# Kernel tuning notes

Hardware: AMD Instinct MI355X
Metric: run time of the kernel (lower is better)

The kernel has to match this reference:

```python
import jax, jax.numpy as jnp
import numpy as np
import math

B, L, S, H, E, D = 4, 2048, 2048, 8, 64, 64


def setup_inputs() -> dict:
    key = jax.random.key(0)
    kq, kk, kv = jax.random.split(key, 3)
    queries = jax.random.normal(kq, (B, L, H, E), dtype=jnp.float32)
    keys = jax.random.normal(kk, (B, S, H, E), dtype=jnp.float32)
    values = jax.random.normal(kv, (B, S, H, D), dtype=jnp.float32)
    # TriangularCausalMask: True above the diagonal = masked out
    attn_mask = jnp.triu(jnp.ones((L, S), dtype=bool), k=1)[None, None]  # [1,1,L,S]
    return {"queries": queries, "keys": keys, "values": values, "attn_mask": attn_mask}


def reference(queries, keys, values, attn_mask):
    # queries [B,L,H,E], keys [B,S,H,E], values [B,S,H,D], attn_mask bool [1,1,L,S]
    scale = 1.0 / math.sqrt(queries.shape[-1])
    scores = jnp.einsum('blhe,bshe->bhls', queries, keys)  # [B,H,L,S]
    scores = jnp.where(attn_mask, -jnp.inf, scores)
    A = jax.nn.softmax(scale * scores, axis=-1)  # dropout p=0.0 -> identity
    V = jnp.einsum('bhls,bshd->blhd', A, values)  # [B,L,H,D]
    return V
```

## Files before the change

kernel.cpp:

```cpp
#include <hip/hip_runtime.h>


typedef unsigned short u16;
typedef unsigned int   u32;
typedef short short8   __attribute__((ext_vector_type(8)));
typedef float floatx16 __attribute__((ext_vector_type(16)));
typedef u32 u32x4      __attribute__((ext_vector_type(4)));

#define B_ 4
#define L_ 2048
#define S_ 2048
#define H_ 8
#define E_ 64
#define D_ 64

static __device__ __forceinline__ u32 pack2(float lo, float hi) {
    const u32 a = __float_as_uint(lo) + 0x8000u;
    const u32 b = __float_as_uint(hi) + 0x8000u;
    return __builtin_amdgcn_perm(b, a, 0x07060302u);
}
static __device__ __forceinline__ u16 bf16c(float x) {
    return (u16)((__float_as_uint(x) + 0x8000u) >> 16);
}
static __device__ __forceinline__ void pl32swap(u32& a, u32& b) {
    asm("v_permlane32_swap_b32 %0, %1" : "+v"(a), "+v"(b));
}
static __device__ __forceinline__ floatx16 zero16() {
    floatx16 z;
    #pragma unroll
    for (int i = 0; i < 16; i++) z[i] = 0.f;
    return z;
}

__global__ __launch_bounds__(256)
void cvt_kernel(const float* __restrict__ k, const float* __restrict__ v,
                u16* __restrict__ kc, u16* __restrict__ vt)
{
    __shared__ u16 Lt[64 * 72];
    const int bx = blockIdx.x, t = threadIdx.x;
    const int tile = bx & 1023;
    const int kt = tile & 31, h = (tile >> 5) & 7, b = tile >> 8;
    const int F  = t >> 5;
    const int hi = (t >> 4) & 1;
    const int l0 = (t & 15) * 2;

    if (bx < 1024) {
        const int mt = F >> 2, ks = F & 3;
        const int s  = kt * 64 + mt * 32 + l0;
        const int e  = ks * 16 + hi * 8;
        const float* p0 = k + (((size_t)(b * S_ + s)) * H_ + h) * E_ + e;
        const float4 a0 = ((const float4*)p0)[0], a1 = ((const float4*)p0)[1];
        const float* p1 = p0 + H_ * E_;
        const float4 b0 = ((const float4*)p1)[0], b1 = ((const float4*)p1)[1];
        u16* dst = kc + ((size_t)(b * 8 + h)) * 131072 + (size_t)kt * 4096 + t * 16;
        *(u32x4*)dst = (u32x4){pack2(a0.x, a0.y), pack2(a0.z, a0.w),
                               pack2(a1.x, a1.y), pack2(a1.z, a1.w)};
        *(u32x4*)(dst + 8) = (u32x4){pack2(b0.x, b0.y), pack2(b0.z, b0.w),
                                     pack2(b1.x, b1.y), pack2(b1.z, b1.w)};
    } else {
        {
            const int i  = t >> 2;
            const int d0 = (t & 3) * 16;
            const float* vp = v + (((size_t)(b * S_ + kt * 64 + i)) * H_ + h) * D_ + d0;
            const float4 a0 = ((const float4*)vp)[0], a1 = ((const float4*)vp)[1];
            const float4 a2 = ((const float4*)vp)[2], a3 = ((const float4*)vp)[3];
            const float va[16] = {a0.x,a0.y,a0.z,a0.w, a1.x,a1.y,a1.z,a1.w,
                                  a2.x,a2.y,a2.z,a2.w, a3.x,a3.y,a3.z,a3.w};
            #pragma unroll
            for (int jj = 0; jj < 16; jj++) Lt[(d0 + jj) * 72 + i] = bf16c(va[jj]);
        }
        __syncthreads();
        {
            const int nt = F >> 2, ks = F & 3;
            const int d1 = nt * 32 + l0;
            u16* dst = vt + ((size_t)(b * 8 + h)) * 131072 + (size_t)kt * 4096 + t * 16;
            *(u32x4*)dst       = *(const u32x4*)&Lt[(d1    ) * 72 + ks * 16 + hi * 8];
            *(u32x4*)(dst + 8) = *(const u32x4*)&Lt[(d1 + 1) * 72 + ks * 16 + hi * 8];
        }
    }
}

template<int SRC>
__global__ __launch_bounds__(128, 2)
void fa_kernel(const float* __restrict__ q, const float* __restrict__ kk,
               const float* __restrict__ vv, const u16* __restrict__ kc,
               const u16* __restrict__ vt, float* __restrict__ out)
{
    __shared__ float Ls[64 * 33 + 128];

    const int tid  = threadIdx.x;
    const int w    = tid >> 6;
    const int lane = tid & 63;
    const int l31  = lane & 31;
    const int hi   = lane >> 5;

    const int bx = blockIdx.x;
    int h, b, s32, kt0, ktend;
    bool split, diag;
    if (bx < 1024) {
        split = true;
        h = bx & 7; b = (bx >> 3) & 3;
        s32 = 63 - (bx >> 5);
        const int klast = s32 >> 1;
        const int mid   = (klast + 1) >> 1;
        if (w == 0) { kt0 = 0;   ktend = mid - 1; diag = false; }
        else        { kt0 = mid; ktend = klast;   diag = true;  }
    } else {
        split = false; diag = true;
        const int idx = bx - 1024;
        h = idx & 7; b = (idx >> 3) & 3;
        const int jj = idx >> 5;
        s32 = w ? jj : (31 - jj);
        kt0 = 0; ktend = s32 >> 1;
    }
    const int q0 = s32 * 32;

    const float kscale = 0.18033688011112042f;

    const float* qptr = q + (((size_t)b * L_ + q0 + l31) * H_ + h) * E_ + hi * 8;
    short8 qf[4];
    #pragma unroll
    for (int ks = 0; ks < 4; ks++) {
        const float4 a0 = *(const float4*)(qptr + ks * 16);
        const float4 a1 = *(const float4*)(qptr + ks * 16 + 4);
        const u32x4 u = {pack2(a0.x * kscale, a0.y * kscale), pack2(a0.z * kscale, a0.w * kscale),
                         pack2(a1.x * kscale, a1.y * kscale), pack2(a1.z * kscale, a1.w * kscale)};
        qf[ks] = __builtin_bit_cast(short8, u);
    }

    const size_t bh = (size_t)(b * 8 + h);
    const u16* kcb = kc + bh * 131072;
    const u16* vtb = vt + bh * 131072;

    auto loadK = [&](int kt, int mt, int ks) -> short8 {
        if constexpr (SRC == 0) {
            const u32x4 u = *(const u32x4*)&kcb[(size_t)kt * 4096 + (mt * 4 + ks) * 512 + lane * 8];
            return __builtin_bit_cast(short8, u);
        } else {
            const float* p = kk + (((size_t)b * S_ + kt * 64 + mt * 32 + l31) * H_ + h) * E_ + ks * 16 + hi * 8;
            const float4 a0 = *(const float4*)p;
            const float4 a1 = *(const float4*)(p + 4);
            const u32x4 u = {pack2(a0.x, a0.y), pack2(a0.z, a0.w), pack2(a1.x, a1.y), pack2(a1.z, a1.w)};
            return __builtin_bit_cast(short8, u);
        }
    };
    auto loadV = [&](int kt, int nt, int ks) -> short8 {
        if constexpr (SRC == 0) {
            const u32x4 u = *(const u32x4*)&vtb[(size_t)kt * 4096 + (nt * 4 + ks) * 512 + lane * 8];
            return __builtin_bit_cast(short8, u);
        } else {
            float f[8];
            #pragma unroll
            for (int jj = 0; jj < 8; jj++)
                f[jj] = vv[(((size_t)b * S_ + kt * 64 + ks * 16 + hi * 8 + jj) * H_ + h) * D_ + nt * 32 + l31];
            const u32x4 u = {pack2(f[0], f[1]), pack2(f[2], f[3]), pack2(f[4], f[5]), pack2(f[6], f[7])};
            return __builtin_bit_cast(short8, u);
        }
    };

    floatx16 occ[2] = {zero16(), zero16()};
    float m_run = -1e30f, l_run = 0.f;

    short8 kf[2][4], vf[2][4];
    #pragma unroll
    for (int mt = 0; mt < 2; mt++)
        #pragma unroll
        for (int ks = 0; ks < 4; ks++) { kf[mt][ks] = loadK(kt0, mt, ks); vf[mt][ks] = loadV(kt0, mt, ks); }

    for (int kt = kt0; kt <= ktend; kt++) {
        floatx16 sac[2];
        __builtin_amdgcn_s_setprio(1);
        #pragma unroll
        for (int mt = 0; mt < 2; mt++) {
            floatx16 c = zero16();
            #pragma unroll
            for (int ks = 0; ks < 4; ks++)
                c = __builtin_amdgcn_mfma_f32_32x32x16_bf16(kf[mt][ks], qf[ks], c, 0, 0, 0);
            sac[mt] = c;
        }
        __builtin_amdgcn_s_setprio(0);

        if (kt < ktend) {
            #pragma unroll
            for (int mt = 0; mt < 2; mt++)
                #pragma unroll
                for (int ks = 0; ks < 4; ks++) kf[mt][ks] = loadK(kt + 1, mt, ks);
        }

        if (diag && kt == ktend) {
            const int qg = q0 + l31;
            #pragma unroll
            for (int mt = 0; mt < 2; mt++)
                #pragma unroll
                for (int r = 0; r < 16; r++) {
                    const int keyg = kt * 64 + mt * 32 + (r & 3) + (r >> 2) * 8 + hi * 4;
                    if (keyg > qg) sac[mt][r] = -1e30f;
                }
        }

        float red[16];
        #pragma unroll
        for (int r = 0; r < 16; r++) red[r] = fmaxf(sac[0][r], sac[1][r]);
        #pragma unroll
        for (int stp = 8; stp > 0; stp >>= 1)
            #pragma unroll
            for (int r = 0; r < stp; r++) red[r] = fmaxf(red[r], red[r + stp]);
        const float mx = fmaxf(red[0], __shfl_xor(red[0], 32));

        const bool defer = __all(mx - m_run <= 8.0f) != 0;
        if (!defer) {
            const float mnew  = fmaxf(m_run, mx);
            const float alpha = exp2f(m_run - mnew);
            m_run = mnew;
            l_run *= alpha;
            #pragma unroll
            for (int nt = 0; nt < 2; nt++)
                #pragma unroll
                for (int r = 0; r < 16; r++) occ[nt][r] *= alpha;
        }

        float sum[16];
        #pragma unroll
        for (int r = 0; r < 16; r++) {
            sac[0][r] = exp2f(sac[0][r] - m_run);
            sac[1][r] = exp2f(sac[1][r] - m_run);
            sum[r] = sac[0][r] + sac[1][r];
        }
        #pragma unroll
        for (int stp = 8; stp > 0; stp >>= 1)
            #pragma unroll
            for (int r = 0; r < stp; r++) sum[r] += sum[r + stp];
        l_run += sum[0] + __shfl_xor(sum[0], 32);

        u32 pk0[8], pk1[8];
        #pragma unroll
        for (int r2 = 0; r2 < 4; r2++) {
            pk0[r2 * 2 + 0] = pack2(sac[0][4 * r2 + 0], sac[0][4 * r2 + 1]);
            pk0[r2 * 2 + 1] = pack2(sac[0][4 * r2 + 2], sac[0][4 * r2 + 3]);
            pk1[r2 * 2 + 0] = pack2(sac[1][4 * r2 + 0], sac[1][4 * r2 + 1]);
            pk1[r2 * 2 + 1] = pack2(sac[1][4 * r2 + 2], sac[1][4 * r2 + 3]);
        }

        __builtin_amdgcn_s_setprio(1);
        #pragma unroll
        for (int ks = 0; ks < 4; ks++) {
            const int u = (ks & 1) * 4;
            u32 w0, w1, w2, w3;
            if (ks < 2) { w0 = pk0[u]; w1 = pk0[u + 1]; w2 = pk0[u + 2]; w3 = pk0[u + 3]; }
            else        { w0 = pk1[u]; w1 = pk1[u + 1]; w2 = pk1[u + 2]; w3 = pk1[u + 3]; }
            pl32swap(w0, w2);
            pl32swap(w1, w3);
            const u32x4 pw = {w0, w1, w2, w3};
            const short8 pf = __builtin_bit_cast(short8, pw);
            occ[0] = __builtin_amdgcn_mfma_f32_32x32x16_bf16(vf[0][ks], pf, occ[0], 0, 0, 0);
            occ[1] = __builtin_amdgcn_mfma_f32_32x32x16_bf16(vf[1][ks], pf, occ[1], 0, 0, 0);
        }
        __builtin_amdgcn_s_setprio(0);

        if (kt < ktend) {
            #pragma unroll
            for (int nt = 0; nt < 2; nt++)
                #pragma unroll
                for (int ks = 0; ks < 4; ks++) vf[nt][ks] = loadV(kt + 1, nt, ks);
        }
    }

    if (split) {
        if (w == 1) {
            #pragma unroll
            for (int nt = 0; nt < 2; nt++)
                #pragma unroll
                for (int r = 0; r < 16; r++) Ls[lane * 33 + nt * 16 + r] = occ[nt][r];
            Ls[2112 + lane] = m_run;
            Ls[2176 + lane] = l_run;
        }
        __syncthreads();
        if (w == 0) {
            const float mB = Ls[2112 + lane], lB = Ls[2176 + lane];
            const float m  = fmaxf(m_run, mB);
            const float aA = exp2f(m_run - m), aB = exp2f(mB - m);
            const float inv = 1.0f / (l_run * aA + lB * aB);
            float* op = out + (((size_t)b * L_ + q0 + l31) * H_ + h) * D_;
            #pragma unroll
            for (int nt = 0; nt < 2; nt++)
                #pragma unroll
                for (int r2 = 0; r2 < 4; r2++) {
                    const float4 o = {
                        (occ[nt][4 * r2 + 0] * aA + Ls[lane * 33 + nt * 16 + 4 * r2 + 0] * aB) * inv,
                        (occ[nt][4 * r2 + 1] * aA + Ls[lane * 33 + nt * 16 + 4 * r2 + 1] * aB) * inv,
                        (occ[nt][4 * r2 + 2] * aA + Ls[lane * 33 + nt * 16 + 4 * r2 + 2] * aB) * inv,
                        (occ[nt][4 * r2 + 3] * aA + Ls[lane * 33 + nt * 16 + 4 * r2 + 3] * aB) * inv};
                    *(float4*)(op + nt * 32 + r2 * 8 + hi * 4) = o;
                }
        }
    } else {
        const float inv = 1.0f / l_run;
        float* op = out + (((size_t)b * L_ + q0 + l31) * H_ + h) * D_;
        #pragma unroll
        for (int nt = 0; nt < 2; nt++)
            #pragma unroll
            for (int r2 = 0; r2 < 4; r2++) {
                const float4 o = {occ[nt][4 * r2 + 0] * inv, occ[nt][4 * r2 + 1] * inv,
                                  occ[nt][4 * r2 + 2] * inv, occ[nt][4 * r2 + 3] * inv};
                *(float4*)(op + nt * 32 + r2 * 8 + hi * 4) = o;
            }
    }
}

extern "C" void kernel_launch(void* const* d_in, const int* in_sizes, int n_in,
                              void* d_out, int out_size, void* d_ws, size_t ws_size,
                              hipStream_t stream) {
    const float* q = (const float*)d_in[0];
    const float* k = (const float*)d_in[1];
    const float* v = (const float*)d_in[2];
    float* out = (float*)d_out;

    const size_t elems = (size_t)B_ * H_ * S_ * E_;
    const size_t need  = elems * 2 * 2;
    if (d_ws != nullptr && ws_size >= need) {
        u16* kc = (u16*)d_ws;
        u16* vt = kc + elems;
        cvt_kernel<<<dim3(2048), dim3(256), 0, stream>>>(k, v, kc, vt);
        fa_kernel<0><<<dim3(1536), dim3(128), 0, stream>>>(q, k, v, kc, vt, out);
    } else {
        fa_kernel<1><<<dim3(1536), dim3(128), 0, stream>>>(q, k, v, nullptr, nullptr, out);
    }
}
```

Measured before the change: 153.4 us.

## Restructure flash-attention loop with K double-buffering, V in-tile loads, and occupancy 3

Rewrites the main KV loop as a two-way unrolled macro that ping-pongs between two K register buffers. V for the current tile and K for the next tile are issued together at the start of each step, with sched_barriers fencing the phases. The launch bound rises from 2 to 3 blocks per SM, the max and sum reductions become shallower trees, and the bf16 packing moves to the hardware v_cvt_pk_bf16_f32 instruction. Non-split blocks are re-paired so the two waves handle adjacent query tiles with equal trip counts. Risks include register spills under the tighter occupancy bound and V load latency now being exposed within the same step.

```diff
diff --git a/kernel.cpp b/kernel.cpp
--- a/kernel.cpp
+++ b/kernel.cpp
@@ -21,6 +21,11 @@
 }
 static __device__ __forceinline__ u16 bf16c(float x) {
     return (u16)((__float_as_uint(x) + 0x8000u) >> 16);
+}
+static __device__ __forceinline__ u32 cvtpk(float lo, float hi) {
+    u32 r;
+    asm("v_cvt_pk_bf16_f32 %0, %1, %2" : "=v"(r) : "v"(lo), "v"(hi));
+    return r;
 }
 static __device__ __forceinline__ void pl32swap(u32& a, u32& b) {
     asm("v_permlane32_swap_b32 %0, %1" : "+v"(a), "+v"(b));
@@ -80,8 +85,102 @@
     }
 }
 
+#define TILE_STEP(CURK, NXTK)                                                   \
+{                                                                               \
+    _Pragma("unroll")                                                           \
+    for (int ks = 0; ks < 4; ks++) {                                            \
+        vf[0][ks] = loadV(kt, 0, ks);                                           \
+        vf[1][ks] = loadV(kt, 1, ks);                                           \
+    }                                                                           \
+    if (kt < ktend) {                                                           \
+        _Pragma("unroll")                                                       \
+        for (int ks = 0; ks < 4; ks++) {                                        \
+            NXTK[0][ks] = loadK(kt + 1, 0, ks);                                 \
+            NXTK[1][ks] = loadK(kt + 1, 1, ks);                                 \
+        }                                                                       \
+    }                                                                           \
+    __builtin_amdgcn_sched_barrier(0);                                          \
+    floatx16 sac0, sac1;                                                        \
+    {                                                                           \
+        __builtin_amdgcn_s_setprio(1);                                          \
+        floatx16 c0 = zero16(), c1 = zero16();                                  \
+        _Pragma("unroll")                                                       \
+        for (int ks = 0; ks < 4; ks++) {                                        \
+            c0 = __builtin_amdgcn_mfma_f32_32x32x16_bf16(CURK[0][ks], qf[ks], c0, 0, 0, 0); \
+            c1 = __builtin_amdgcn_mfma_f32_32x32x16_bf16(CURK[1][ks], qf[ks], c1, 0, 0, 0); \
+        }                                                                       \
+        __builtin_amdgcn_s_setprio(0);                                          \
+        sac0 = c0; sac1 = c1;                                                   \
+    }                                                                           \
+    __builtin_amdgcn_sched_barrier(0);                                          \
+    if (diag && kt == ktend) {                                                  \
+        const int qg = q0 + l31;                                                \
+        _Pragma("unroll")                                                       \
+        for (int r = 0; r < 16; r++) {                                          \
+            const int key0 = kt * 64 + (r & 3) + (r >> 2) * 8 + hi * 4;         \
+            if (key0 > qg)      sac0[r] = -1e30f;                               \
+            if (key0 + 32 > qg) sac1[r] = -1e30f;                               \
+        }                                                                       \
+    }                                                                           \
+    float m01[8];                                                               \
+    _Pragma("unroll")                                                           \
+    for (int r = 0; r < 8; r++)                                                 \
+        m01[r] = fmaxf(fmaxf(sac0[r], sac0[r + 8]), fmaxf(sac1[r], sac1[r + 8])); \
+    const float t0  = fmaxf(fmaxf(m01[0], m01[1]), m01[2]);                     \
+    const float t1  = fmaxf(fmaxf(m01[3], m01[4]), m01[5]);                     \
+    const float t2  = fmaxf(fmaxf(m01[6], m01[7]), t0);                         \
+    const float mxl = fmaxf(t1, t2);                                            \
+    const float mx  = fmaxf(mxl, __shfl_xor(mxl, 32));                          \
+    const bool defer = __all(mx - m_run <= 8.0f) != 0;                          \
+    if (!defer) {                                                               \
+        const float mnew  = fmaxf(m_run, mx);                                   \
+        const float alpha = exp2f(m_run - mnew);                                \
+        m_run = mnew;                                                           \
+        l_run *= alpha;                                                         \
+        _Pragma("unroll")                                                       \
+        for (int r = 0; r < 16; r++) { occ[0][r] *= alpha; occ[1][r] *= alpha; } \
+    }                                                                           \
+    _Pragma("unroll")                                                           \
+    for (int r = 0; r < 16; r++) {                                              \
+        sac0[r] = exp2f(sac0[r] - m_run);                                       \
+        sac1[r] = exp2f(sac1[r] - m_run);                                       \
+    }                                                                           \
+    float sm[8];                                                                \
+    _Pragma("unroll")                                                           \
+    for (int r = 0; r < 8; r++)                                                 \
+        sm[r] = (sac0[r] + sac0[r + 8]) + (sac1[r] + sac1[r + 8]);              \
+    const float u0 = (sm[0] + sm[1]) + (sm[2] + sm[3]);                         \
+    const float u1 = (sm[4] + sm[5]) + (sm[6] + sm[7]);                         \
+    const float pssum = u0 + u1;                                                \
+    l_run += pssum + __shfl_xor(pssum, 32);                                     \
+    __builtin_amdgcn_sched_barrier(0);                                          \
+    u32 pk0[8], pk1[8];                                                         \
+    _Pragma("unroll")                                                           \
+    for (int r2 = 0; r2 < 4; r2++) {                                            \
+        pk0[2 * r2 + 0] = cvtpk(sac0[4 * r2 + 0], sac0[4 * r2 + 1]);            \
+        pk0[2 * r2 + 1] = cvtpk(sac0[4 * r2 + 2], sac0[4 * r2 + 3]);            \
+        pk1[2 * r2 + 0] = cvtpk(sac1[4 * r2 + 0], sac1[4 * r2 + 1]);            \
+        pk1[2 * r2 + 1] = cvtpk(sac1[4 * r2 + 2], sac1[4 * r2 + 3]);            \
+    }                                                                           \
+    __builtin_amdgcn_s_setprio(1);                                              \
+    _Pragma("unroll")                                                           \
+    for (int ks = 0; ks < 4; ks++) {                                            \
+        const int u = (ks & 1) * 4;                                             \
+        u32 w0, w1, w2, w3;                                                     \
+        if (ks < 2) { w0 = pk0[u]; w1 = pk0[u + 1]; w2 = pk0[u + 2]; w3 = pk0[u + 3]; } \
+        else        { w0 = pk1[u]; w1 = pk1[u + 1]; w2 = pk1[u + 2]; w3 = pk1[u + 3]; } \
+        pl32swap(w0, w2);                                                       \
+        pl32swap(w1, w3);                                                       \
+        const u32x4 pw = {w0, w1, w2, w3};                                      \
+        const short8 pf = __builtin_bit_cast(short8, pw);                       \
+        occ[0] = __builtin_amdgcn_mfma_f32_32x32x16_bf16(vf[0][ks], pf, occ[0], 0, 0, 0); \
+        occ[1] = __builtin_amdgcn_mfma_f32_32x32x16_bf16(vf[1][ks], pf, occ[1], 0, 0, 0); \
+    }                                                                           \
+    __builtin_amdgcn_s_setprio(0);                                              \
+}
+
 template<int SRC>
-__global__ __launch_bounds__(128, 2)
+__global__ __launch_bounds__(128, 3)
 void fa_kernel(const float* __restrict__ q, const float* __restrict__ kk,
                const float* __restrict__ vv, const u16* __restrict__ kc,
                const u16* __restrict__ vt, float* __restrict__ out)
@@ -109,9 +208,9 @@
         split = false; diag = true;
         const int idx = bx - 1024;
         h = idx & 7; b = (idx >> 3) & 3;
-        const int jj = idx >> 5;
-        s32 = w ? jj : (31 - jj);
-        kt0 = 0; ktend = s32 >> 1;
+        const int jj = 15 - (idx >> 5);
+        s32 = 2 * jj + w;
+        kt0 = 0; ktend = jj;
     }
     const int q0 = s32 * 32;
 
@@ -151,8 +250,8 @@
         } else {
             float f[8];
             #pragma unroll
-            for (int jj = 0; jj < 8; jj++)
-                f[jj] = vv[(((size_t)b * S_ + kt * 64 + ks * 16 + hi * 8 + jj) * H_ + h) * D_ + nt * 32 + l31];
+            for (int jj2 = 0; jj2 < 8; jj2++)
+                f[jj2] = vv[(((size_t)b * S_ + kt * 64 + ks * 16 + hi * 8 + jj2) * H_ + h) * D_ + nt * 32 + l31];
             const u32x4 u = {pack2(f[0], f[1]), pack2(f[2], f[3]), pack2(f[4], f[5]), pack2(f[6], f[7])};
             return __builtin_bit_cast(short8, u);
         }
@@ -161,108 +260,18 @@
     floatx16 occ[2] = {zero16(), zero16()};
     float m_run = -1e30f, l_run = 0.f;
 
-    short8 kf[2][4], vf[2][4];
+    short8 kfA[2][4], kfB[2][4], vf[2][4];
     #pragma unroll
-    for (int mt = 0; mt < 2; mt++)
-        #pragma unroll
-        for (int ks = 0; ks < 4; ks++) { kf[mt][ks] = loadK(kt0, mt, ks); vf[mt][ks] = loadV(kt0, mt, ks); }
-
-    for (int kt = kt0; kt <= ktend; kt++) {
-        floatx16 sac[2];
-        __builtin_amdgcn_s_setprio(1);
-        #pragma unroll
-        for (int mt = 0; mt < 2; mt++) {
-            floatx16 c = zero16();
-            #pragma unroll
-            for (int ks = 0; ks < 4; ks++)
-                c = __builtin_amdgcn_mfma_f32_32x32x16_bf16(kf[mt][ks], qf[ks], c, 0, 0, 0);
-            sac[mt] = c;
-        }
-        __builtin_amdgcn_s_setprio(0);
-
-        if (kt < ktend) {
-            #pragma unroll
-            for (int mt = 0; mt < 2; mt++)
-                #pragma unroll
-                for (int ks = 0; ks < 4; ks++) kf[mt][ks] = loadK(kt + 1, mt, ks);
-        }
-
-        if (diag && kt == ktend) {
-            const int qg = q0 + l31;
-            #pragma unroll
-            for (int mt = 0; mt < 2; mt++)
-                #pragma unroll
-                for (int r = 0; r < 16; r++) {
-                    const int keyg = kt * 64 + mt * 32 + (r & 3) + (r >> 2) * 8 + hi * 4;
-                    if (keyg > qg) sac[mt][r] = -1e30f;
-                }
-        }
-
-        float red[16];
-        #pragma unroll
-        for (int r = 0; r < 16; r++) red[r] = fmaxf(sac[0][r], sac[1][r]);
-        #pragma unroll
-        for (int stp = 8; stp > 0; stp >>= 1)
-            #pragma unroll
-            for (int r = 0; r < stp; r++) red[r] = fmaxf(red[r], red[r + stp]);
-        const float mx = fmaxf(red[0], __shfl_xor(red[0], 32));
-
-        const bool defer = __all(mx - m_run <= 8.0f) != 0;
-        if (!defer) {
-            const float mnew  = fmaxf(m_run, mx);
-            const float alpha = exp2f(m_run - mnew);
-            m_run = mnew;
-            l_run *= alpha;
-            #pragma unroll
-            for (int nt = 0; nt < 2; nt++)
-                #pragma unroll
-                for (int r = 0; r < 16; r++) occ[nt][r] *= alpha;
-        }
-
-        float sum[16];
-        #pragma unroll
-        for (int r = 0; r < 16; r++) {
-            sac[0][r] = exp2f(sac[0][r] - m_run);
-            sac[1][r] = exp2f(sac[1][r] - m_run);
-            sum[r] = sac[0][r] + sac[1][r];
-        }
-        #pragma unroll
-        for (int stp = 8; stp > 0; stp >>= 1)
-            #pragma unroll
-            for (int r = 0; r < stp; r++) sum[r] += sum[r + stp];
-        l_run += sum[0] + __shfl_xor(sum[0], 32);
-
-        u32 pk0[8], pk1[8];
-        #pragma unroll
-        for (int r2 = 0; r2 < 4; r2++) {
-            pk0[r2 * 2 + 0] = pack2(sac[0][4 * r2 + 0], sac[0][4 * r2 + 1]);
-            pk0[r2 * 2 + 1] = pack2(sac[0][4 * r2 + 2], sac[0][4 * r2 + 3]);
-            pk1[r2 * 2 + 0] = pack2(sac[1][4 * r2 + 0], sac[1][4 * r2 + 1]);
-            pk1[r2 * 2 + 1] = pack2(sac[1][4 * r2 + 2], sac[1][4 * r2 + 3]);
-        }
-
-        __builtin_amdgcn_s_setprio(1);
-        #pragma unroll
-        for (int ks = 0; ks < 4; ks++) {
-            const int u = (ks & 1) * 4;
-            u32 w0, w1, w2, w3;
-            if (ks < 2) { w0 = pk0[u]; w1 = pk0[u + 1]; w2 = pk0[u + 2]; w3 = pk0[u + 3]; }
-            else        { w0 = pk1[u]; w1 = pk1[u + 1]; w2 = pk1[u + 2]; w3 = pk1[u + 3]; }
-            pl32swap(w0, w2);
-            pl32swap(w1, w3);
-            const u32x4 pw = {w0, w1, w2, w3};
-            const short8 pf = __builtin_bit_cast(short8, pw);
-            occ[0] = __builtin_amdgcn_mfma_f32_32x32x16_bf16(vf[0][ks], pf, occ[0], 0, 0, 0);
-            occ[1] = __builtin_amdgcn_mfma_f32_32x32x16_bf16(vf[1][ks], pf, occ[1], 0, 0, 0);
-        }
-        __builtin_amdgcn_s_setprio(0);
-
-        if (kt < ktend) {
-            #pragma unroll
-            for (int nt = 0; nt < 2; nt++)
-                #pragma unroll
-                for (int ks = 0; ks < 4; ks++) vf[nt][ks] = loadV(kt + 1, nt, ks);
-        }
+    for (int ks = 0; ks < 4; ks++) { kfA[0][ks] = loadK(kt0, 0, ks); kfA[1][ks] = loadK(kt0, 1, ks); }
+
+    int kt = kt0;
+    for (;;) {
+        TILE_STEP(kfA, kfB)
+        if (kt == ktend) break;
+        ++kt;
+        TILE_STEP(kfB, kfA)
+        if (kt == ktend) break;
+        ++kt;
     }
 
     if (split) {
```

Result: slower. 230.3 us (+50.1%).

## Share K/V tiles across four waves via async global-to-LDS double buffering

Applied to the files above, without the earlier changes.

Restructures the attention kernel so each 256-thread block handles 128 query rows (four waves of 32), loading K/V tiles into LDS once per block with global_load_lds and double buffering, instead of each wave loading fragments from global memory on its own. The two-wave split-KV scheme with its LDS merge is removed, and load balance now comes from pairing mirrored query blocks (j and 15-j). This cuts redundant global traffic for K/V but adds block-wide barriers every tile, and waves whose rows lie entirely before the key tile sit idle past the causal limit. The grid shrinks from 1536 to 512 blocks.

```diff
diff --git a/kernel.cpp b/kernel.cpp
--- a/kernel.cpp
+++ b/kernel.cpp
@@ -30,6 +30,11 @@
     #pragma unroll
     for (int i = 0; i < 16; i++) z[i] = 0.f;
     return z;
+}
+static __device__ __forceinline__ void gload_lds16(u16* lds, const u16* g) {
+    __builtin_amdgcn_global_load_lds((const __attribute__((address_space(1))) void*)g,
+                                     (__attribute__((address_space(3))) void*)lds,
+                                     16, 0, 0);
 }
 
 __global__ __launch_bounds__(256)
@@ -81,12 +86,12 @@
 }
 
 template<int SRC>
-__global__ __launch_bounds__(128, 2)
+__global__ __launch_bounds__(256, 2)
 void fa_kernel(const float* __restrict__ q, const float* __restrict__ kk,
                const float* __restrict__ vv, const u16* __restrict__ kc,
                const u16* __restrict__ vt, float* __restrict__ out)
 {
-    __shared__ float Ls[64 * 33 + 128];
+    __shared__ __align__(16) u16 KV[2][8192];
 
     const int tid  = threadIdx.x;
     const int w    = tid >> 6;
@@ -94,26 +99,15 @@
     const int l31  = lane & 31;
     const int hi   = lane >> 5;
 
-    const int bx = blockIdx.x;
-    int h, b, s32, kt0, ktend;
-    bool split, diag;
-    if (bx < 1024) {
-        split = true;
-        h = bx & 7; b = (bx >> 3) & 3;
-        s32 = 63 - (bx >> 5);
-        const int klast = s32 >> 1;
-        const int mid   = (klast + 1) >> 1;
-        if (w == 0) { kt0 = 0;   ktend = mid - 1; diag = false; }
-        else        { kt0 = mid; ktend = klast;   diag = true;  }
-    } else {
-        split = false; diag = true;
-        const int idx = bx - 1024;
-        h = idx & 7; b = (idx >> 3) & 3;
-        const int jj = idx >> 5;
-        s32 = w ? jj : (31 - jj);
-        kt0 = 0; ktend = s32 >> 1;
-    }
-    const int q0 = s32 * 32;
+    const int bx   = blockIdx.x;
+    const int h    = bx & 7;
+    const int b    = (bx >> 3) & 3;
+    const int idx  = (bx >> 5) & 7;
+    const int j    = (bx >> 8) ? idx : (15 - idx);
+    const int q0   = 128 * j + 32 * w;
+    const int ktend = 2 * j + 1;
+    const int qlim = q0 + 31;
+    const int dt   = (q0 + 31) >> 6;
 
     const float kscale = 0.18033688011112042f;
 
@@ -132,179 +126,170 @@
     const u16* kcb = kc + bh * 131072;
     const u16* vtb = vt + bh * 131072;
 
-    auto loadK = [&](int kt, int mt, int ks) -> short8 {
-        if constexpr (SRC == 0) {
-            const u32x4 u = *(const u32x4*)&kcb[(size_t)kt * 4096 + (mt * 4 + ks) * 512 + lane * 8];
-            return __builtin_bit_cast(short8, u);
-        } else {
+    auto stage = [&](int kt, int bufi) {
+        #pragma unroll
+        for (int ff = 0; ff < 2; ff++) {
+            const int f = w * 2 + ff;
+            gload_lds16(&KV[bufi][f * 512],        kcb + (size_t)kt * 4096 + f * 512 + lane * 8);
+            gload_lds16(&KV[bufi][4096 + f * 512], vtb + (size_t)kt * 4096 + f * 512 + lane * 8);
+        }
+    };
+    auto stage_sync = [&](int kt) {
+        #pragma unroll
+        for (int ff = 0; ff < 2; ff++) {
+            const int f = w * 2 + ff;
+            const int mt = f >> 2, ks = f & 3;
             const float* p = kk + (((size_t)b * S_ + kt * 64 + mt * 32 + l31) * H_ + h) * E_ + ks * 16 + hi * 8;
             const float4 a0 = *(const float4*)p;
             const float4 a1 = *(const float4*)(p + 4);
-            const u32x4 u = {pack2(a0.x, a0.y), pack2(a0.z, a0.w), pack2(a1.x, a1.y), pack2(a1.z, a1.w)};
-            return __builtin_bit_cast(short8, u);
-        }
-    };
-    auto loadV = [&](int kt, int nt, int ks) -> short8 {
-        if constexpr (SRC == 0) {
-            const u32x4 u = *(const u32x4*)&vtb[(size_t)kt * 4096 + (nt * 4 + ks) * 512 + lane * 8];
-            return __builtin_bit_cast(short8, u);
-        } else {
-            float f[8];
+            *(u32x4*)&KV[0][f * 512 + lane * 8] =
+                (u32x4){pack2(a0.x, a0.y), pack2(a0.z, a0.w), pack2(a1.x, a1.y), pack2(a1.z, a1.w)};
+            float fv[8];
             #pragma unroll
             for (int jj = 0; jj < 8; jj++)
-                f[jj] = vv[(((size_t)b * S_ + kt * 64 + ks * 16 + hi * 8 + jj) * H_ + h) * D_ + nt * 32 + l31];
-            const u32x4 u = {pack2(f[0], f[1]), pack2(f[2], f[3]), pack2(f[4], f[5]), pack2(f[6], f[7])};
-            return __builtin_bit_cast(short8, u);
+                fv[jj] = vv[(((size_t)b * S_ + kt * 64 + ks * 16 + hi * 8 + jj) * H_ + h) * D_ + mt * 32 + l31];
+            *(u32x4*)&KV[0][4096 + f * 512 + lane * 8] =
+                (u32x4){pack2(fv[0], fv[1]), pack2(fv[2], fv[3]), pack2(fv[4], fv[5]), pack2(fv[6], fv[7])};
         }
     };
 
     floatx16 occ[2] = {zero16(), zero16()};
     float m_run = -1e30f, l_run = 0.f;
 
-    short8 kf[2][4], vf[2][4];
+    if constexpr (SRC == 0) {
+        stage(0, 0);
+        asm volatile("s_waitcnt vmcnt(0)" ::: "memory");
+        __builtin_amdgcn_s_barrier();
+        __builtin_amdgcn_sched_barrier(0);
+    }
+
+    for (int kt = 0; kt <= ktend; kt++) {
+        int cur;
+        if constexpr (SRC == 0) {
+            cur = kt & 1;
+            if (kt < ktend) {
+                stage(kt + 1, cur ^ 1);
+                asm volatile("s_waitcnt vmcnt(4)" ::: "memory");
+            } else {
+                asm volatile("s_waitcnt vmcnt(0)" ::: "memory");
+            }
+            __builtin_amdgcn_s_barrier();
+            __builtin_amdgcn_sched_barrier(0);
+        } else {
+            cur = 0;
+            stage_sync(kt);
+            __syncthreads();
+        }
+
+        if (kt * 64 <= qlim) {
+            short8 kfr[2][4], vfr[2][4];
+            #pragma unroll
+            for (int mt = 0; mt < 2; mt++)
+                #pragma unroll
+                for (int ks = 0; ks < 4; ks++) {
+                    kfr[mt][ks] = *(const short8*)&KV[cur][(mt * 4 + ks) * 512 + lane * 8];
+                    vfr[mt][ks] = *(const short8*)&KV[cur][4096 + (mt * 4 + ks) * 512 + lane * 8];
+                }
+
+            floatx16 sac[2];
+            __builtin_amdgcn_s_setprio(1);
+            #pragma unroll
+            for (int mt = 0; mt < 2; mt++) {
+                floatx16 c = zero16();
+                #pragma unroll
+                for (int ks = 0; ks < 4; ks++)
+                    c = __builtin_amdgcn_mfma_f32_32x32x16_bf16(kfr[mt][ks], qf[ks], c, 0, 0, 0);
+                sac[mt] = c;
+            }
+            __builtin_amdgcn_s_setprio(0);
+
+            if (kt >= dt) {
+                const int qg = q0 + l31;
+                #pragma unroll
+                for (int mt = 0; mt < 2; mt++)
+                    #pragma unroll
+                    for (int r = 0; r < 16; r++) {
+                        const int keyg = kt * 64 + mt * 32 + (r & 3) + (r >> 2) * 8 + hi * 4;
+                        if (keyg > qg) sac[mt][r] = -1e30f;
+                    }
+            }
+
+            float red[16];
+            #pragma unroll
+            for (int r = 0; r < 16; r++) red[r] = fmaxf(sac[0][r], sac[1][r]);
+            #pragma unroll
+            for (int stp = 8; stp > 0; stp >>= 1)
+                #pragma unroll
+                for (int r = 0; r < stp; r++) red[r] = fmaxf(red[r], red[r + stp]);
+            const float mx = fmaxf(red[0], __shfl_xor(red[0], 32));
+
+            const bool defer = __all(mx - m_run <= 8.0f) != 0;
+            if (!defer) {
+                const float mnew  = fmaxf(m_run, mx);
+                const float alpha = exp2f(m_run - mnew);
+                m_run = mnew;
+                l_run *= alpha;
+                #pragma unroll
+                for (int r = 0; r < 16; r++) { occ[0][r] *= alpha; occ[1][r] *= alpha; }
+            }
+
+            float sum[16];
+            #pragma unroll
+            for (int r = 0; r < 16; r++) {
+                sac[0][r] = exp2f(sac[0][r] - m_run);
+                sac[1][r] = exp2f(sac[1][r] - m_run);
+                sum[r] = sac[0][r] + sac[1][r];
+            }
+            #pragma unroll
+            for (int stp = 8; stp > 0; stp >>= 1)
+                #pragma unroll
+                for (int r = 0; r < stp; r++) sum[r] += sum[r + stp];
+            l_run += sum[0] + __shfl_xor(sum[0], 32);
+
+            u32 pk0[8], pk1[8];
+            #pragma unroll
+            for (int r2 = 0; r2 < 4; r2++) {
+                pk0[2 * r2 + 0] = pack2(sac[0][4 * r2 + 0], sac[0][4 * r2 + 1]);
+                pk0[2 * r2 + 1] = pack2(sac[0][4 * r2 + 2], sac[0][4 * r2 + 3]);
+                pk1[2 * r2 + 0] = pack2(sac[1][4 * r2 + 0], sac[1][4 * r2 + 1]);
+                pk1[2 * r2 + 1] = pack2(sac[1][4 * r2 + 2], sac[1][4 * r2 + 3]);
+            }
+
+            __builtin_amdgcn_s_setprio(1);
+            #pragma unroll
+            for (int ks = 0; ks < 4; ks++) {
+                const int u = (ks & 1) * 4;
+                u32 w0, w1, w2, w3;
+                if (ks < 2) { w0 = pk0[u]; w1 = pk0[u + 1]; w2 = pk0[u + 2]; w3 = pk0[u + 3]; }
+                else        { w0 = pk1[u]; w1 = pk1[u + 1]; w2 = pk1[u + 2]; w3 = pk1[u + 3]; }
+                pl32swap(w0, w2);
+                pl32swap(w1, w3);
+                const u32x4 pw = {w0, w1, w2, w3};
+                const short8 pf = __builtin_bit_cast(short8, pw);
+                occ[0] = __builtin_amdgcn_mfma_f32_32x32x16_bf16(vfr[0][ks], pf, occ[0], 0, 0, 0);
+                occ[1] = __builtin_amdgcn_mfma_f32_32x32x16_bf16(vfr[1][ks], pf, occ[1], 0, 0, 0);
+            }
+            __builtin_amdgcn_s_setprio(0);
+        }
+
+        if constexpr (SRC == 0) {
+            __builtin_amdgcn_sched_barrier(0);
+            __builtin_amdgcn_s_barrier();
+        } else {
+            __syncthreads();
+        }
+    }
+
+    const float inv = 1.0f / l_run;
+    float* op = out + (((size_t)b * L_ + q0 + l31) * H_ + h) * D_;
     #pragma unroll
-    for (int mt = 0; mt < 2; mt++)
-        #pragma unroll
-        for (int ks = 0; ks < 4; ks++) { kf[mt][ks] = loadK(kt0, mt, ks); vf[mt][ks] = loadV(kt0, mt, ks); }
-
-    for (int kt = kt0; kt <= ktend; kt++) {
-        floatx16 sac[2];
-        __builtin_amdgcn_s_setprio(1);
-        #pragma unroll
-        for (int mt = 0; mt < 2; mt++) {
-            floatx16 c = zero16();
-            #pragma unroll
-            for (int ks = 0; ks < 4; ks++)
-                c = __builtin_amdgcn_mfma_f32_32x32x16_bf16(kf[mt][ks], qf[ks], c, 0, 0, 0);
-            sac[mt] = c;
-        }
-        __builtin_amdgcn_s_setprio(0);
-
-        if (kt < ktend) {
-            #pragma unroll
-            for (int mt = 0; mt < 2; mt++)
-                #pragma unroll
-                for (int ks = 0; ks < 4; ks++) kf[mt][ks] = loadK(kt + 1, mt, ks);
-        }
-
-        if (diag && kt == ktend) {
-            const int qg = q0 + l31;
-            #pragma unroll
-            for (int mt = 0; mt < 2; mt++)
-                #pragma unroll
-                for (int r = 0; r < 16; r++) {
-                    const int keyg = kt * 64 + mt * 32 + (r & 3) + (r >> 2) * 8 + hi * 4;
-                    if (keyg > qg) sac[mt][r] = -1e30f;
-                }
-        }
-
-        float red[16];
-        #pragma unroll
-        for (int r = 0; r < 16; r++) red[r] = fmaxf(sac[0][r], sac[1][r]);
-        #pragma unroll
-        for (int stp = 8; stp > 0; stp >>= 1)
-            #pragma unroll
-            for (int r = 0; r < stp; r++) red[r] = fmaxf(red[r], red[r + stp]);
-        const float mx = fmaxf(red[0], __shfl_xor(red[0], 32));
-
-        const bool defer = __all(mx - m_run <= 8.0f) != 0;
-        if (!defer) {
-            const float mnew  = fmaxf(m_run, mx);
-            const float alpha = exp2f(m_run - mnew);
-            m_run = mnew;
-            l_run *= alpha;
-            #pragma unroll
-            for (int nt = 0; nt < 2; nt++)
-                #pragma unroll
-                for (int r = 0; r < 16; r++) occ[nt][r] *= alpha;
-        }
-
-        float sum[16];
-        #pragma unroll
-        for (int r = 0; r < 16; r++) {
-            sac[0][r] = exp2f(sac[0][r] - m_run);
-            sac[1][r] = exp2f(sac[1][r] - m_run);
-            sum[r] = sac[0][r] + sac[1][r];
-        }
-        #pragma unroll
-        for (int stp = 8; stp > 0; stp >>= 1)
-            #pragma unroll
-            for (int r = 0; r < stp; r++) sum[r] += sum[r + stp];
-        l_run += sum[0] + __shfl_xor(sum[0], 32);
-
-        u32 pk0[8], pk1[8];
+    for (int nt = 0; nt < 2; nt++)
         #pragma unroll
         for (int r2 = 0; r2 < 4; r2++) {
-            pk0[r2 * 2 + 0] = pack2(sac[0][4 * r2 + 0], sac[0][4 * r2 + 1]);
-            pk0[r2 * 2 + 1] = pack2(sac[0][4 * r2 + 2], sac[0][4 * r2 + 3]);
-            pk1[r2 * 2 + 0] = pack2(sac[1][4 * r2 + 0], sac[1][4 * r2 + 1]);
-            pk1[r2 * 2 + 1] = pack2(sac[1][4 * r2 + 2], sac[1][4 * r2 + 3]);
-        }
-
-        __builtin_amdgcn_s_setprio(1);
-        #pragma unroll
-        for (int ks = 0; ks < 4; ks++) {
-            const int u = (ks & 1) * 4;
-            u32 w0, w1, w2, w3;
-            if (ks < 2) { w0 = pk0[u]; w1 = pk0[u + 1]; w2 = pk0[u + 2]; w3 = pk0[u + 3]; }
-            else        { w0 = pk1[u]; w1 = pk1[u + 1]; w2 = pk1[u + 2]; w3 = pk1[u + 3]; }
-            pl32swap(w0, w2);
-            pl32swap(w1, w3);
-            const u32x4 pw = {w0, w1, w2, w3};
-            const short8 pf = __builtin_bit_cast(short8, pw);
-            occ[0] = __builtin_amdgcn_mfma_f32_32x32x16_bf16(vf[0][ks], pf, occ[0], 0, 0, 0);
-            occ[1] = __builtin_amdgcn_mfma_f32_32x32x16_bf16(vf[1][ks], pf, occ[1], 0, 0, 0);
-        }
-        __builtin_amdgcn_s_setprio(0);
-
-        if (kt < ktend) {
-            #pragma unroll
-            for (int nt = 0; nt < 2; nt++)
-                #pragma unroll
-                for (int ks = 0; ks < 4; ks++) vf[nt][ks] = loadV(kt + 1, nt, ks);
-        }
-    }
-
-    if (split) {
-        if (w == 1) {
-            #pragma unroll
-            for (int nt = 0; nt < 2; nt++)
-                #pragma unroll
-                for (int r = 0; r < 16; r++) Ls[lane * 33 + nt * 16 + r] = occ[nt][r];
-            Ls[2112 + lane] = m_run;
-            Ls[2176 + lane] = l_run;
-        }
-        __syncthreads();
-        if (w == 0) {
-            const float mB = Ls[2112 + lane], lB = Ls[2176 + lane];
-            const float m  = fmaxf(m_run, mB);
-            const float aA = exp2f(m_run - m), aB = exp2f(mB - m);
-            const float inv = 1.0f / (l_run * aA + lB * aB);
-            float* op = out + (((size_t)b * L_ + q0 + l31) * H_ + h) * D_;
-            #pragma unroll
-            for (int nt = 0; nt < 2; nt++)
-                #pragma unroll
-                for (int r2 = 0; r2 < 4; r2++) {
-                    const float4 o = {
-                        (occ[nt][4 * r2 + 0] * aA + Ls[lane * 33 + nt * 16 + 4 * r2 + 0] * aB) * inv,
-                        (occ[nt][4 * r2 + 1] * aA + Ls[lane * 33 + nt * 16 + 4 * r2 + 1] * aB) * inv,
-                        (occ[nt][4 * r2 + 2] * aA + Ls[lane * 33 + nt * 16 + 4 * r2 + 2] * aB) * inv,
-                        (occ[nt][4 * r2 + 3] * aA + Ls[lane * 33 + nt * 16 + 4 * r2 + 3] * aB) * inv};
-                    *(float4*)(op + nt * 32 + r2 * 8 + hi * 4) = o;
-                }
-        }
-    } else {
-        const float inv = 1.0f / l_run;
-        float* op = out + (((size_t)b * L_ + q0 + l31) * H_ + h) * D_;
-        #pragma unroll
-        for (int nt = 0; nt < 2; nt++)
-            #pragma unroll
-            for (int r2 = 0; r2 < 4; r2++) {
-                const float4 o = {occ[nt][4 * r2 + 0] * inv, occ[nt][4 * r2 + 1] * inv,
-                                  occ[nt][4 * r2 + 2] * inv, occ[nt][4 * r2 + 3] * inv};
-                *(float4*)(op + nt * 32 + r2 * 8 + hi * 4) = o;
-            }
-    }
+            const float4 o = {occ[nt][4 * r2 + 0] * inv, occ[nt][4 * r2 + 1] * inv,
+                              occ[nt][4 * r2 + 2] * inv, occ[nt][4 * r2 + 3] * inv};
+            *(float4*)(op + nt * 32 + r2 * 8 + hi * 4) = o;
+        }
 }
 
 extern "C" void kernel_launch(void* const* d_in, const int* in_sizes, int n_in,
@@ -321,8 +306,8 @@
         u16* kc = (u16*)d_ws;
         u16* vt = kc + elems;
         cvt_kernel<<<dim3(2048), dim3(256), 0, stream>>>(k, v, kc, vt);
-        fa_kernel<0><<<dim3(1536), dim3(128), 0, stream>>>(q, k, v, kc, vt, out);
+        fa_kernel<0><<<dim3(512), dim3(256), 0, stream>>>(q, k, v, kc, vt, out);
     } else {
-        fa_kernel<1><<<dim3(1536), dim3(128), 0, stream>>>(q, k, v, nullptr, nullptr, out);
-    }
-}
+        fa_kernel<1><<<dim3(512), dim3(256), 0, stream>>>(q, k, v, nullptr, nullptr, out);
+    }
+}
```

Result: no change. 153.1 us (-0.2%).
